# Performance work log

Hardware: AMD Instinct MI355X
Metric: run time of the kernel (lower is better)

Reference implementation:

```python
import jax, jax.numpy as jnp
import numpy as np


def setup_inputs() -> dict:
    key = jax.random.key(0)
    k1, k2 = jax.random.split(key)
    B, C, N = 128, 3, 320
    G = N * N
    inp = jax.random.normal(k1, (B, C, G), dtype=jnp.float32)
    tgt = jax.random.randint(k2, (B, G), 0, C, dtype=jnp.int64)
    return {"input": inp, "target": tgt}


def reference(input, target):
    B, C, G = input.shape
    N = int(round(np.sqrt(G)))
    # strict upper-triangle edge indices (offset=1), static under jit
    iu0, iu1 = np.triu_indices(N, k=1)
    # gather upper-triangle entries: [B, C, E] and [B, E]
    triu_input = input.reshape(B, C, N, N)[:, :, iu0, iu1]
    triu_target = target.reshape(B, N, N)[:, iu0, iu1]
    triu_preds = jnp.argmax(triu_input, axis=1)  # [B, E]
    edge_acc = (triu_preds == triu_target).astype(jnp.float32).mean()
    return 1.0 - edge_acc
```

## Files before the change

kernel.cpp:

```cpp
#include <hip/hip_runtime.h>

constexpr int B    = 128;
constexpr int C    = 3;
constexpr int N    = 320;
constexpr int G    = N * N;
constexpr int G4   = G / 4;
constexpr int ROW4 = N / 4;
constexpr unsigned long long TOTAL_EDGES =
    (unsigned long long)B * (unsigned long long)(N * (N - 1) / 2);

__global__ __launch_bounds__(256) void edge_acc_kernel(
    const float* __restrict__ inp,
    const int*   __restrict__ tgt,
    unsigned int* __restrict__ counter)
{
    const int nChunks = B * G4;
    const int tid     = blockIdx.x * blockDim.x + threadIdx.x;
    const int stride  = gridDim.x * blockDim.x;

    unsigned int cnt = 0;

    for (int cid = tid; cid < nChunks; cid += stride) {
        const int b  = cid / G4;
        const int q  = cid - b * G4;
        const int i  = q / ROW4;
        const int jb = (q - i * ROW4) * 4;

        if (jb + 3 <= i) continue;

        const size_t plane = (size_t)b * C * G;
        const size_t gofs  = (size_t)q * 4;

        const float4 x0 = *(const float4*)(inp + plane            + gofs);
        const float4 x1 = *(const float4*)(inp + plane + (size_t)G     + gofs);
        const float4 x2 = *(const float4*)(inp + plane + (size_t)2 * G + gofs);
        const int4   tv = *(const int4*)(tgt + (size_t)b * G + gofs);

        {
            int pred = 0; float m = x0.x;
            if (x1.x > m) { m = x1.x; pred = 1; }
            if (x2.x > m) { pred = 2; }
            cnt += (unsigned)((jb + 0 > i) & (pred == tv.x));
        }
        {
            int pred = 0; float m = x0.y;
            if (x1.y > m) { m = x1.y; pred = 1; }
            if (x2.y > m) { pred = 2; }
            cnt += (unsigned)((jb + 1 > i) & (pred == tv.y));
        }
        {
            int pred = 0; float m = x0.z;
            if (x1.z > m) { m = x1.z; pred = 1; }
            if (x2.z > m) { pred = 2; }
            cnt += (unsigned)((jb + 2 > i) & (pred == tv.z));
        }
        {
            int pred = 0; float m = x0.w;
            if (x1.w > m) { m = x1.w; pred = 1; }
            if (x2.w > m) { pred = 2; }
            cnt += (unsigned)((jb + 3 > i) & (pred == tv.w));
        }
    }

    #pragma unroll
    for (int off = 32; off > 0; off >>= 1)
        cnt += __shfl_down(cnt, off, 64);

    __shared__ unsigned int wsum[4];
    const int lane = threadIdx.x & 63;
    const int wave = threadIdx.x >> 6;
    if (lane == 0) wsum[wave] = cnt;
    __syncthreads();

    if (threadIdx.x == 0) {
        unsigned int s = wsum[0] + wsum[1] + wsum[2] + wsum[3];
        if (s) atomicAdd(counter, s);
    }
}

__global__ void finalize_kernel(const unsigned int* __restrict__ counter,
                                float* __restrict__ out)
{
    const double acc = (double)counter[0] / (double)TOTAL_EDGES;
    out[0] = 1.0f - (float)acc;
}

extern "C" void kernel_launch(void* const* d_in, const int* in_sizes, int n_in,
                              void* d_out, int out_size, void* d_ws, size_t ws_size,
                              hipStream_t stream) {
    const float* inp = (const float*)d_in[0];
    const int*   tgt = (const int*)d_in[1];
    float*       out = (float*)d_out;
    unsigned int* counter = (unsigned int*)d_ws;

    hipMemsetAsync(counter, 0, sizeof(unsigned int), stream);

    const int threads = 256;
    const int blocks  = 2048;
    edge_acc_kernel<<<blocks, threads, 0, stream>>>(inp, tgt, counter);
    finalize_kernel<<<1, 1, 0, stream>>>(counter, out);
}
```

Baseline: 241.3 us.

## Map threads to fixed positions across batches and replace atomic with partial sums

Each thread now owns one spatial 4-element chunk and iterates over a fixed set of batches with an unrolled loop, hoisting index math and triangle masks out of the loop and exposing multiple independent loads. The global atomic and memset are replaced by per-block partial writes reduced by a parallel finalize kernel. Threads entirely below the diagonal exit immediately, leaving some idle lanes in exchange for less per-iteration overhead.

```diff
diff --git a/kernel.cpp b/kernel.cpp
--- a/kernel.cpp
+++ b/kernel.cpp
@@ -6,59 +6,66 @@
 constexpr int G    = N * N;
 constexpr int G4   = G / 4;
 constexpr int ROW4 = N / 4;
+constexpr int BLOCKS  = 3200;
+constexpr int THREADS = 256;
+constexpr int BSTEP   = (BLOCKS * THREADS) / G4;
+constexpr int ITERS   = B / BSTEP;
 constexpr unsigned long long TOTAL_EDGES =
     (unsigned long long)B * (unsigned long long)(N * (N - 1) / 2);
 
-__global__ __launch_bounds__(256) void edge_acc_kernel(
+__global__ __launch_bounds__(THREADS) void edge_acc_kernel(
     const float* __restrict__ inp,
     const int*   __restrict__ tgt,
-    unsigned int* __restrict__ counter)
+    unsigned int* __restrict__ partials)
 {
-    const int nChunks = B * G4;
-    const int tid     = blockIdx.x * blockDim.x + threadIdx.x;
-    const int stride  = gridDim.x * blockDim.x;
+    const int tid = blockIdx.x * THREADS + threadIdx.x;
+    const int q   = tid % G4;
+    const int b0  = tid / G4;
+    const int i   = q / ROW4;
+    const int jb  = (q - i * ROW4) * 4;
 
     unsigned int cnt = 0;
 
-    for (int cid = tid; cid < nChunks; cid += stride) {
-        const int b  = cid / G4;
-        const int q  = cid - b * G4;
-        const int i  = q / ROW4;
-        const int jb = (q - i * ROW4) * 4;
+    if (jb + 3 > i) {
+        const unsigned m0 = (unsigned)(jb + 0 > i);
+        const unsigned m1 = (unsigned)(jb + 1 > i);
+        const unsigned m2 = (unsigned)(jb + 2 > i);
+        const size_t gofs = (size_t)q * 4;
 
-        if (jb + 3 <= i) continue;
+        #pragma unroll
+        for (int it = 0; it < ITERS; ++it) {
+            const int b = b0 + BSTEP * it;
+            const float* p = inp + (size_t)b * (C * G) + gofs;
 
-        const size_t plane = (size_t)b * C * G;
-        const size_t gofs  = (size_t)q * 4;
+            const float4 x0 = *(const float4*)(p);
+            const float4 x1 = *(const float4*)(p + G);
+            const float4 x2 = *(const float4*)(p + 2 * G);
+            const int4   tv = *(const int4*)(tgt + (size_t)b * G + gofs);
 
-        const float4 x0 = *(const float4*)(inp + plane            + gofs);
-        const float4 x1 = *(const float4*)(inp + plane + (size_t)G     + gofs);
-        const float4 x2 = *(const float4*)(inp + plane + (size_t)2 * G + gofs);
-        const int4   tv = *(const int4*)(tgt + (size_t)b * G + gofs);
-
-        {
-            int pred = 0; float m = x0.x;
-            if (x1.x > m) { m = x1.x; pred = 1; }
-            if (x2.x > m) { pred = 2; }
-            cnt += (unsigned)((jb + 0 > i) & (pred == tv.x));
-        }
-        {
-            int pred = 0; float m = x0.y;
-            if (x1.y > m) { m = x1.y; pred = 1; }
-            if (x2.y > m) { pred = 2; }
-            cnt += (unsigned)((jb + 1 > i) & (pred == tv.y));
-        }
-        {
-            int pred = 0; float m = x0.z;
-            if (x1.z > m) { m = x1.z; pred = 1; }
-            if (x2.z > m) { pred = 2; }
-            cnt += (unsigned)((jb + 2 > i) & (pred == tv.z));
-        }
-        {
-            int pred = 0; float m = x0.w;
-            if (x1.w > m) { m = x1.w; pred = 1; }
-            if (x2.w > m) { pred = 2; }
-            cnt += (unsigned)((jb + 3 > i) & (pred == tv.w));
+            {
+                int pred = 0; float m = x0.x;
+                if (x1.x > m) { m = x1.x; pred = 1; }
+                if (x2.x > m) { pred = 2; }
+                cnt += m0 & (unsigned)(pred == tv.x);
+            }
+            {
+                int pred = 0; float m = x0.y;
+                if (x1.y > m) { m = x1.y; pred = 1; }
+                if (x2.y > m) { pred = 2; }
+                cnt += m1 & (unsigned)(pred == tv.y);
+            }
+            {
+                int pred = 0; float m = x0.z;
+                if (x1.z > m) { m = x1.z; pred = 1; }
+                if (x2.z > m) { pred = 2; }
+                cnt += m2 & (unsigned)(pred == tv.z);
+            }
+            {
+                int pred = 0; float m = x0.w;
+                if (x1.w > m) { m = x1.w; pred = 1; }
+                if (x2.w > m) { pred = 2; }
+                cnt += (unsigned)(pred == tv.w);
+            }
         }
     }
 
@@ -66,23 +73,38 @@
     for (int off = 32; off > 0; off >>= 1)
         cnt += __shfl_down(cnt, off, 64);
 
-    __shared__ unsigned int wsum[4];
+    __shared__ unsigned int wsum[THREADS / 64];
     const int lane = threadIdx.x & 63;
     const int wave = threadIdx.x >> 6;
     if (lane == 0) wsum[wave] = cnt;
     __syncthreads();
 
-    if (threadIdx.x == 0) {
-        unsigned int s = wsum[0] + wsum[1] + wsum[2] + wsum[3];
-        if (s) atomicAdd(counter, s);
-    }
+    if (threadIdx.x == 0)
+        partials[blockIdx.x] = wsum[0] + wsum[1] + wsum[2] + wsum[3];
 }
 
-__global__ void finalize_kernel(const unsigned int* __restrict__ counter,
-                                float* __restrict__ out)
+__global__ __launch_bounds__(256) void finalize_kernel(
+    const unsigned int* __restrict__ partials,
+    float* __restrict__ out)
 {
-    const double acc = (double)counter[0] / (double)TOTAL_EDGES;
-    out[0] = 1.0f - (float)acc;
+    unsigned int s = 0;
+    for (int idx = threadIdx.x; idx < BLOCKS; idx += 256)
+        s += partials[idx];
+
+    #pragma unroll
+    for (int off = 32; off > 0; off >>= 1)
+        s += __shfl_down(s, off, 64);
+
+    __shared__ unsigned int wsum[4];
+    const int lane = threadIdx.x & 63;
+    const int wave = threadIdx.x >> 6;
+    if (lane == 0) wsum[wave] = s;
+    __syncthreads();
+
+    if (threadIdx.x == 0) {
+        const unsigned int total = wsum[0] + wsum[1] + wsum[2] + wsum[3];
+        out[0] = 1.0f - (float)((double)total / (double)TOTAL_EDGES);
+    }
 }
 
 extern "C" void kernel_launch(void* const* d_in, const int* in_sizes, int n_in,
@@ -91,12 +113,8 @@
     const float* inp = (const float*)d_in[0];
     const int*   tgt = (const int*)d_in[1];
     float*       out = (float*)d_out;
-    unsigned int* counter = (unsigned int*)d_ws;
+    unsigned int* partials = (unsigned int*)d_ws;
 
-    hipMemsetAsync(counter, 0, sizeof(unsigned int), stream);
-
-    const int threads = 256;
-    const int blocks  = 2048;
-    edge_acc_kernel<<<blocks, threads, 0, stream>>>(inp, tgt, counter);
-    finalize_kernel<<<1, 1, 0, stream>>>(counter, out);
+    edge_acc_kernel<<<BLOCKS, THREADS, 0, stream>>>(inp, tgt, partials);
+    finalize_kernel<<<1, 256, 0, stream>>>(partials, out);
 }
```

After: 236.7 us. About the same (-1.9%).
